# Kernel optimization log

Measured on AMD Instinct MI355X. Metric: run time of the kernel, lower is better.

Reference implementation:

```python
import jax, jax.numpy as jnp
import numpy as np

N, E, G, H, C, DIN, DE = 20000, 320000, 32, 8, 56, 32, 5
HC = H * C  # 448
NEG_SLOPE = 0.2
EPS_BN = 1e-5


def _seg_softmax(scores, seg, num):
    # scores: [E, H], softmax over edges sharing the same target node
    m = jax.ops.segment_max(scores, seg, num_segments=num)
    e = jnp.exp(scores - m[seg])
    s = jax.ops.segment_sum(e, seg, num_segments=num)
    return e / (s[seg] + 1e-16)


def _add_self_loops(src, dst, eattr, n):
    # PyG fill_value='mean': self-loop edge_attr = mean of incoming edge_attr
    deg = jax.ops.segment_sum(jnp.ones((src.shape[0],), eattr.dtype), dst, num_segments=n)
    esum = jax.ops.segment_sum(eattr, dst, num_segments=n)
    loop_attr = esum / jnp.maximum(deg, 1.0)[:, None]
    ar = jnp.arange(n, dtype=src.dtype)
    return (jnp.concatenate([src, ar]), jnp.concatenate([dst, ar]),
            jnp.concatenate([eattr, loop_attr], axis=0))


def _gatv2(x, src, dst, eattr, Wl, Wr, We, att, bias, n):
    xl = (x @ Wl).reshape(n, H, C)  # source transform (messages)
    xr = (x @ Wr).reshape(n, H, C)  # target transform
    ee = (eattr @ We).reshape(-1, H, C)
    s = jax.nn.leaky_relu(xl[src] + xr[dst] + ee, NEG_SLOPE)  # [E, H, C]
    score = jnp.einsum('ehc,hc->eh', s, att)
    alpha = _seg_softmax(score, dst, n)
    out = jax.ops.segment_sum(alpha[..., None] * xl[src], dst, num_segments=n)
    return out.reshape(n, HC) + bias


def _bn(x, gamma, beta):
    m = x.mean(axis=0)
    v = x.var(axis=0)  # biased variance, as torch BatchNorm1d (training)
    return (x - m) * jax.lax.rsqrt(v + EPS_BN) * gamma + beta


def setup_inputs() -> dict:
    key = jax.random.key(0)
    ks = jax.random.split(key, 18)
    sc = lambda k, shape: (jax.random.normal(k, shape, jnp.float32) * 0.05)
    return {
        'x': jax.random.normal(ks[0], (N, DIN), jnp.float32),
        'edge_index': jax.random.randint(ks[1], (2, E), 0, N),
        'edge_attr': jax.random.normal(ks[2], (E, DE), jnp.float32),
        'batch': jnp.sort(jax.random.randint(ks[3], (N,), 0, G)),
        'Wl1': sc(ks[4], (DIN, HC)), 'Wr1': sc(ks[5], (DIN, HC)),
        'We1': sc(ks[6], (DE, HC)), 'att1': sc(ks[7], (H, C)),
        'bias1': jnp.zeros((HC,), jnp.float32),
        'Wl2': sc(ks[8], (HC, HC)), 'Wr2': sc(ks[9], (HC, HC)),
        'We2': sc(ks[10], (DE, HC)), 'att2': sc(ks[11], (H, C)),
        'bias2': jnp.zeros((HC,), jnp.float32),
        'bn_gamma': jnp.ones((HC,), jnp.float32),
        'bn_beta': jnp.zeros((HC,), jnp.float32),
        'Wlin': sc(ks[12], (HC, 18)),
        'blin': jnp.zeros((18,), jnp.float32),
    }


def reference(x, edge_index, edge_attr, batch, Wl1, Wr1, We1, att1, bias1,
              Wl2, Wr2, We2, att2, bias2, bn_gamma, bn_beta, Wlin, blin):
    src, dst = edge_index[0], edge_index[1]
    src2, dst2, ea2 = _add_self_loops(src, dst, edge_attr, N)
    # dropout is identity in eval
    h = _gatv2(x, src2, dst2, ea2, Wl1, Wr1, We1, att1, bias1, N)
    h = jax.nn.elu(h)
    h = _bn(h, bn_gamma, bn_beta)
    h = _gatv2(h, src2, dst2, ea2, Wl2, Wr2, We2, att2, bias2, N)
    # global mean pool per graph
    cnt = jax.ops.segment_sum(jnp.ones((N,), h.dtype), batch, num_segments=G)
    pooled = jax.ops.segment_sum(h, batch, num_segments=G) / jnp.maximum(cnt, 1.0)[:, None]
    pooled = _bn(pooled, bn_gamma, bn_beta)
    logits = pooled @ Wlin + blin
    return jax.nn.log_softmax(logits, axis=1)
```

## Files before the change

kernel.cpp:

```cpp
#include <hip/hip_runtime.h>
#include <hip/hip_bf16.h>

#define NN   20000
#define EE   320000
#define EN   340000
#define HH   8
#define CC   56
#define HC   448
#define DEA  5
#define EAS  8
#define DINN 32
#define GG   32
#define NEG  0.2f

#define SS   896
#define MT   157
#define NT   7

typedef short bf16x8 __attribute__((ext_vector_type(8)));
typedef float f32x4  __attribute__((ext_vector_type(4)));
typedef float f32x8  __attribute__((ext_vector_type(8)));

static __device__ __forceinline__ unsigned short f2bf(float f) {
  unsigned int u = __float_as_uint(f);
  u += 0x7fffu + ((u >> 16) & 1u);
  return (unsigned short)(u >> 16);
}

static __device__ __forceinline__ f32x8 bf8_to_f32x8(uint4 u) {
  f32x8 o;
  o[0] = __uint_as_float(u.x << 16); o[1] = __uint_as_float(u.x & 0xffff0000u);
  o[2] = __uint_as_float(u.y << 16); o[3] = __uint_as_float(u.y & 0xffff0000u);
  o[4] = __uint_as_float(u.z << 16); o[5] = __uint_as_float(u.z & 0xffff0000u);
  o[6] = __uint_as_float(u.w << 16); o[7] = __uint_as_float(u.w & 0xffff0000u);
  return o;
}

static __device__ __forceinline__ float dpp8_sum(float x) {
  int v = __float_as_int(x);
  x += __int_as_float(__builtin_amdgcn_update_dpp(0, v, 0xB1, 0xF, 0xF, true));
  v = __float_as_int(x);
  x += __int_as_float(__builtin_amdgcn_update_dpp(0, v, 0x4E, 0xF, 0xF, true));
  v = __float_as_int(x);
  x += __int_as_float(__builtin_amdgcn_update_dpp(0, v, 0x141, 0xF, 0xF, true));
  return x;
}

__global__ void k_deg(const int* __restrict__ dst, int* deg) {
  int e = blockIdx.x * 256 + threadIdx.x;
  if (e < EE) atomicAdd(&deg[dst[e]], 1);
}

__global__ __launch_bounds__(1024) void k_scan(const int* __restrict__ deg, int* offs,
                                               int* cursor) {
  __shared__ int tot[1024];
  int t = threadIdx.x;
  int base = t * 20;
  int loc[20];
  int s = 0;
  #pragma unroll
  for (int i = 0; i < 20; i++) {
    int idx = base + i;
    int v = (idx < NN) ? deg[idx] + 1 : 0;
    loc[i] = s;
    s += v;
  }
  tot[t] = s;
  __syncthreads();
  for (int o = 1; o < 1024; o <<= 1) {
    int v = (t >= o) ? tot[t - o] : 0;
    __syncthreads();
    tot[t] += v;
    __syncthreads();
  }
  int basesum = (t == 0) ? 0 : tot[t - 1];
  #pragma unroll
  for (int i = 0; i < 20; i++) {
    int idx = base + i;
    if (idx < NN) { offs[idx] = basesum + loc[i]; cursor[idx] = basesum + loc[i]; }
  }
  if (t == 1023) offs[NN] = tot[1023];
}

__global__ void k_scatter(const int* __restrict__ src, const int* __restrict__ dst,
                          const float* __restrict__ ea,
                          int* cursor, int* __restrict__ csr_src, float* __restrict__ csr_ea) {
  int i = blockIdx.x * 256 + threadIdx.x;
  if (i >= EE) return;
  int d = dst[i], s = src[i];
  float a[DEA];
  #pragma unroll
  for (int j = 0; j < DEA; j++) a[j] = ea[(size_t)i * DEA + j];
  int pos = atomicAdd(&cursor[d], 1);
  csr_src[pos] = s;
  float* o = csr_ea + (size_t)pos * EAS;
  *(f32x4*)o       = (f32x4){a[0], a[1], a[2], a[3]};
  *(f32x4*)(o + 4) = (f32x4){a[4], 0.f, 0.f, 0.f};
}

#define XCN (NN * DINN)
#define W1N (SS * DINN)
#define W2N (SS * HC)
__global__ void k_aux(const int* __restrict__ offs,
                      int* __restrict__ csr_src, float* __restrict__ csr_ea,
                      const float* __restrict__ x, unsigned short* __restrict__ xb,
                      const float* __restrict__ Wl1, const float* __restrict__ Wr1,
                      unsigned short* __restrict__ W1t,
                      const float* __restrict__ Wl2, const float* __restrict__ Wr2,
                      unsigned short* __restrict__ W2t) {
  int i = blockIdx.x * 256 + threadIdx.x;
  if (i < NN) {
    int n = i;
    int e0 = offs[n], e1 = offs[n + 1] - 1;
    float a0 = 0.f, a1 = 0.f, a2 = 0.f, a3 = 0.f, a4 = 0.f;
    for (int e = e0; e < e1; e++) {
      const float* p = csr_ea + (size_t)e * EAS;
      a0 += p[0]; a1 += p[1]; a2 += p[2]; a3 += p[3]; a4 += p[4];
    }
    float inv = 1.f / fmaxf((float)(e1 - e0), 1.f);
    csr_src[e1] = n;
    float* o = csr_ea + (size_t)e1 * EAS;
    *(f32x4*)o       = (f32x4){a0 * inv, a1 * inv, a2 * inv, a3 * inv};
    *(f32x4*)(o + 4) = (f32x4){a4 * inv, 0.f, 0.f, 0.f};
    return;
  }
  i -= NN;
  if (i < XCN) { xb[i] = f2bf(x[i]); return; }
  i -= XCN;
  if (i < W1N) {
    int col = i / DINN, k = i - col * DINN;
    int cc = (col < HC) ? col : col - HC;
    const float* W = (col < HC) ? Wl1 : Wr1;
    W1t[i] = f2bf(W[(size_t)k * HC + cc]);
    return;
  }
  i -= W1N;
  if (i < W2N) {
    int col = i / HC, k = i - col * HC;
    int cc = (col < HC) ? col : col - HC;
    const float* W = (col < HC) ? Wl2 : Wr2;
    W2t[i] = f2bf(W[(size_t)k * HC + cc]);
  }
}

__global__ __launch_bounds__(256) void k_gemm1(const unsigned short* __restrict__ xb,
                                               const unsigned short* __restrict__ W1t,
                                               unsigned short* __restrict__ out) {
  int w = threadIdx.x >> 6, lane = threadIdx.x & 63;
  int q = lane >> 4, r = lane & 15;
  int m0 = blockIdx.x * 64;
  int node = blockIdx.y * 64 + w * 16 + r;
  int nc = node < NN ? node : NN - 1;
  bf16x8 b = *(const bf16x8*)(xb + (size_t)nc * DINN + q * 8);
  #pragma unroll
  for (int j = 0; j < 4; j++) {
    bf16x8 a = *(const bf16x8*)(W1t + (size_t)(m0 + j * 16 + r) * DINN + q * 8);
    f32x4 acc = {0.f, 0.f, 0.f, 0.f};
    acc = __builtin_amdgcn_mfma_f32_16x16x32_bf16(a, b, acc, 0, 0, 0);
    uint2 st;
    st.x = ((unsigned int)f2bf(acc[1]) << 16) | f2bf(acc[0]);
    st.y = ((unsigned int)f2bf(acc[3]) << 16) | f2bf(acc[2]);
    if (node < NN)
      *(uint2*)(out + (size_t)node * SS + m0 + j * 16 + q * 4) = st;
  }
}

__global__ __launch_bounds__(256) void k_attn(
    const unsigned short* __restrict__ xlr,
    const int* __restrict__ offs, const int* __restrict__ csr_src,
    const float* __restrict__ csr_ea,
    const float* __restrict__ We, const float* __restrict__ att,
    const float* __restrict__ bias,
    unsigned short* __restrict__ outb, float* __restrict__ outf, int layer1) {
  int n = __builtin_amdgcn_readfirstlane(blockIdx.x * 4 + (threadIdx.x >> 6));
  if (n >= NN) return;
  int lane = threadIdx.x & 63;
  int head = lane >> 3, sub = lane & 7;
  bool v = sub < 7;
  int cb = head * 56 + (v ? sub : 6) * 8;

  f32x8 z = {0.f,0.f,0.f,0.f,0.f,0.f,0.f,0.f};
  f32x8 xr = bf8_to_f32x8(*(const uint4*)(xlr + (size_t)n * SS + HC + cb));
  f32x8 at = *(const f32x8*)(att + cb);
  if (!v) at = z;
  f32x8 w0 = *(const f32x8*)(We + 0 * HC + cb);
  f32x8 w1 = *(const f32x8*)(We + 1 * HC + cb);
  f32x8 w2 = *(const f32x8*)(We + 2 * HC + cb);
  f32x8 w3 = *(const f32x8*)(We + 3 * HC + cb);
  f32x8 w4 = *(const f32x8*)(We + 4 * HC + cb);

  int e0 = offs[n], e1 = offs[n + 1];
  int last = e1 - 1;
  float l = 0.f;
  f32x8 acc = z;

  int s_cur[4];
  #pragma unroll
  for (int k = 0; k < 4; k++) {
    int ek = e0 + k; ek = ek < last ? ek : last;
    s_cur[k] = csr_src[__builtin_amdgcn_readfirstlane(ek)];
  }

  for (int e = e0; e < e1; e += 4) {
    uint4 g[4];
    #pragma unroll
    for (int k = 0; k < 4; k++)
      g[k] = *(const uint4*)(xlr + (size_t)s_cur[k] * SS + cb);

    int en = e + 4;
    if (en < e1) {
      #pragma unroll
      for (int k = 0; k < 4; k++) {
        int ek = en + k; ek = ek < last ? ek : last;
        s_cur[k] = csr_src[__builtin_amdgcn_readfirstlane(ek)];
      }
    }

    f32x8 md[4];
    #pragma unroll
    for (int k = 0; k < 4; k++) {
      int ek = e + k; ek = ek < last ? ek : last;
      md[k] = *(const f32x8*)(csr_ea + (size_t)__builtin_amdgcn_readfirstlane(ek) * EAS);
    }

    #pragma unroll
    for (int k = 0; k < 4; k++) {
      f32x8 tb = xr;
      tb += md[k][0] * w0; tb += md[k][1] * w1; tb += md[k][2] * w2;
      tb += md[k][3] * w3; tb += md[k][4] * w4;
      f32x8 xl = bf8_to_f32x8(g[k]);
      f32x8 t = tb + xl;
      #pragma unroll
      for (int i = 0; i < 8; i++) t[i] = fmaxf(t[i], NEG * t[i]);
      float p = 0.f;
      #pragma unroll
      for (int i = 0; i < 8; i++) p += t[i] * at[i];
      p = dpp8_sum(p);
      float wv = (e + k < e1) ? __expf(fminf(p, 60.f)) : 0.f;
      acc += wv * xl;
      l += wv;
    }
  }

  f32x8 b8 = *(const f32x8*)(bias + cb);
  f32x8 o = acc * (1.f / (l + 1e-16f)) + b8;
  if (layer1) {
    if (v) {
      #pragma unroll
      for (int i = 0; i < 8; i++) o[i] = o[i] > 0.f ? o[i] : (__expf(o[i]) - 1.f);
      uint4 pk;
      pk.x = ((unsigned int)f2bf(o[1]) << 16) | f2bf(o[0]);
      pk.y = ((unsigned int)f2bf(o[3]) << 16) | f2bf(o[2]);
      pk.z = ((unsigned int)f2bf(o[5]) << 16) | f2bf(o[4]);
      pk.w = ((unsigned int)f2bf(o[7]) << 16) | f2bf(o[6]);
      *(uint4*)(outb + (size_t)n * HC + cb) = pk;
    }
  } else if (v) {
    float* dst = outf + (size_t)n * HC + cb;
    *(f32x4*)dst       = (f32x4){o[0], o[1], o[2], o[3]};
    *(f32x4*)(dst + 4) = (f32x4){o[4], o[5], o[6], o[7]};
  }
}

__global__ __launch_bounds__(448) void k_bnstats(const unsigned short* __restrict__ h,
                                                 float* stat) {
  int c = threadIdx.x;
  int rows_per = (NN + gridDim.x - 1) / gridDim.x;
  int r0 = blockIdx.x * rows_per, r1 = min(NN, r0 + rows_per);
  float s = 0.f, sq = 0.f;
  for (int r = r0; r < r1; r++) {
    unsigned int u = h[(size_t)r * HC + c];
    float v = __uint_as_float(u << 16);
    s += v; sq += v * v;
  }
  atomicAdd(&stat[c], s);
  atomicAdd(&stat[HC + c], sq);
}

__global__ __launch_bounds__(64) void k_w2fix(const unsigned short* __restrict__ W2t,
                                              const float* __restrict__ stat,
                                              const float* __restrict__ gam,
                                              const float* __restrict__ bet,
                                              unsigned short* __restrict__ W2s,
                                              float* __restrict__ bias2) {
  int j = blockIdx.x;
  int t = threadIdx.x;
  float bacc = 0.f;
  #pragma unroll
  for (int it = 0; it < 7; it++) {
    int k = t + it * 64;
    float w = __uint_as_float((unsigned int)W2t[(size_t)j * HC + k] << 16);
    float mean = stat[k] * (1.f / NN);
    float var  = stat[HC + k] * (1.f / NN) - mean * mean;
    float sc = rsqrtf(var + 1e-5f) * gam[k];
    float sh = bet[k] - mean * sc;
    bacc += sh * w;
    W2s[(size_t)j * HC + k] = f2bf(sc * w);
  }
  #pragma unroll
  for (int m = 32; m >= 1; m >>= 1) bacc += __shfl_xor(bacc, m, 64);
  if (t == 0) bias2[j] = bacc;
}

__global__ __launch_bounds__(256) void k_gemm2(const unsigned short* __restrict__ A,
                                               const unsigned short* __restrict__ Bt,
                                               const float* __restrict__ bias2,
                                               unsigned short* __restrict__ out) {
  __shared__ unsigned short As[128 * 64];
  __shared__ unsigned short Bs[128 * 64];
  int bid = blockIdx.x;
  int g = bid / 56, rem = bid - g * 56;
  int xs = min(8, MT - g * 8);
  int bx = g * 8 + rem % xs;
  int by = rem / xs;
  int t = threadIdx.x;
  int w = t >> 6, lane = t & 63;
  int wm = w >> 1, wn = w & 1;
  int q = lane >> 4, r = lane & 15;
  int m0 = bx * 128;
  int n0 = by * 128;

  const unsigned short *ag[4], *bg[4];
  unsigned short *la[4], *lb[4];
  #pragma unroll
  for (int j = 0; j < 4; j++) {
    int s = t + j * 256;
    int row = s >> 3;
    int gcol = (s & 7) ^ (row & 7);
    int ar = m0 + row; if (ar >= NN) ar = NN - 1;
    ag[j] = A + (size_t)ar * HC + gcol * 8;
    bg[j] = Bt + (size_t)(n0 + row) * HC + gcol * 8;
    la[j] = As + s * 8;
    lb[j] = Bs + s * 8;
  }

  f32x4 zero = {0.f, 0.f, 0.f, 0.f};
  f32x4 acc[4][4];
  #pragma unroll
  for (int i = 0; i < 4; i++)
    #pragma unroll
    for (int j = 0; j < 4; j++) acc[i][j] = zero;

  for (int k0 = 0; k0 < HC; k0 += 64) {
    #pragma unroll
    for (int j = 0; j < 4; j++) {
      __builtin_amdgcn_global_load_lds(
          (const __attribute__((address_space(1))) unsigned int*)(ag[j] + k0),
          (__attribute__((address_space(3))) unsigned int*)la[j], 16, 0, 0);
      __builtin_amdgcn_global_load_lds(
          (const __attribute__((address_space(1))) unsigned int*)(bg[j] + k0),
          (__attribute__((address_space(3))) unsigned int*)lb[j], 16, 0, 0);
    }
    __syncthreads();
    #pragma unroll
    for (int kk = 0; kk < 64; kk += 32) {
      int p = (kk >> 3) + q;
      bf16x8 af[4], bf[4];
      #pragma unroll
      for (int i = 0; i < 4; i++) {
        int row = wm * 64 + i * 16 + r;
        af[i] = *(const bf16x8*)(As + row * 64 + ((p ^ (r & 7)) * 8));
      }
      #pragma unroll
      for (int j = 0; j < 4; j++) {
        int row = wn * 64 + j * 16 + r;
        bf[j] = *(const bf16x8*)(Bs + row * 64 + ((p ^ (r & 7)) * 8));
      }
      #pragma unroll
      for (int i = 0; i < 4; i++)
        #pragma unroll
        for (int j = 0; j < 4; j++)
          acc[i][j] = __builtin_amdgcn_mfma_f32_16x16x32_bf16(af[i], bf[j], acc[i][j], 0, 0, 0);
    }
    __syncthreads();
  }

  #pragma unroll
  for (int j = 0; j < 4; j++) {
    int col = n0 + wn * 64 + j * 16 + r;
    float bs = bias2[col];
    #pragma unroll
    for (int i = 0; i < 4; i++) {
      int row_base = m0 + wm * 64 + i * 16 + q * 4;
      #pragma unroll
      for (int reg = 0; reg < 4; reg++) {
        int row = row_base + reg;
        if (row < NN) out[(size_t)row * SS + col] = f2bf(acc[i][j][reg] + bs);
      }
    }
  }
}

__global__ __launch_bounds__(448) void k_pool(const float* __restrict__ h2,
                                              const int* __restrict__ batch,
                                              float* pooled, int* cnt) {
  int c = threadIdx.x;
  int rows_per = (NN + gridDim.x - 1) / gridDim.x;
  int r0 = blockIdx.x * rows_per, r1 = min(NN, r0 + rows_per);
  if (r0 >= r1) return;
  float loc = 0.f;
  int rc = 0;
  int gcur = batch[r0];
  for (int r = r0; r < r1; r++) {
    int g = batch[r];
    if (g != gcur) {
      atomicAdd(&pooled[gcur * HC + c], loc);
      if (c == 0) atomicAdd(&cnt[gcur], rc);
      loc = 0.f; rc = 0; gcur = g;
    }
    loc += h2[(size_t)r * HC + c];
    rc++;
  }
  atomicAdd(&pooled[gcur * HC + c], loc);
  if (c == 0) atomicAdd(&cnt[gcur], rc);
}

__global__ __launch_bounds__(448) void k_final(const float* __restrict__ pooled_sum,
                                               const int* __restrict__ cnt,
                                               const float* __restrict__ gam,
                                               const float* __restrict__ bet,
                                               const float* __restrict__ Wlin,
                                               const float* __restrict__ blin,
                                               float* __restrict__ out) {
  __shared__ float P[GG * HC];
  __shared__ float L[GG * 18];
  __shared__ float red[GG];
  int c = threadIdx.x;
  float s = 0.f, sq = 0.f;
  for (int g = 0; g < GG; g++) {
    float v = pooled_sum[g * HC + c] / fmaxf((float)cnt[g], 1.f);
    P[g * HC + c] = v; s += v; sq += v * v;
  }
  float mean = s * (1.f / GG);
  float var  = sq * (1.f / GG) - mean * mean;
  float sc = rsqrtf(var + 1e-5f) * gam[c];
  float sh = bet[c] - mean * sc;
  for (int g = 0; g < GG; g++) P[g * HC + c] = P[g * HC + c] * sc + sh;
  __syncthreads();
  for (int o = c; o < GG * 18; o += HC) {
    int g = o / 18, j = o - g * 18;
    float acc = blin[j];
    for (int k = 0; k < HC; k++) acc += P[g * HC + k] * Wlin[k * 18 + j];
    L[o] = acc;
  }
  __syncthreads();
  if (c < GG) {
    float mx = -3.4e38f;
    for (int j = 0; j < 18; j++) mx = fmaxf(mx, L[c * 18 + j]);
    float se = 0.f;
    for (int j = 0; j < 18; j++) se += __expf(L[c * 18 + j] - mx);
    red[c] = mx + logf(se);
  }
  __syncthreads();
  for (int o = c; o < GG * 18; o += HC) out[o] = L[o] - red[o / 18];
}

extern "C" void kernel_launch(void* const* d_in, const int* in_sizes, int n_in,
                              void* d_out, int out_size, void* d_ws, size_t ws_size,
                              hipStream_t stream) {
  (void)in_sizes; (void)n_in; (void)out_size; (void)ws_size;
  const float* x     = (const float*)d_in[0];
  const int*   ei    = (const int*)d_in[1];
  const float* ea    = (const float*)d_in[2];
  const int*   batch = (const int*)d_in[3];
  const float* Wl1   = (const float*)d_in[4];
  const float* Wr1   = (const float*)d_in[5];
  const float* We1   = (const float*)d_in[6];
  const float* att1  = (const float*)d_in[7];
  const float* bias1 = (const float*)d_in[8];
  const float* Wl2   = (const float*)d_in[9];
  const float* Wr2   = (const float*)d_in[10];
  const float* We2   = (const float*)d_in[11];
  const float* att2  = (const float*)d_in[12];
  const float* bias2in = (const float*)d_in[13];
  const float* gam   = (const float*)d_in[14];
  const float* bet   = (const float*)d_in[15];
  const float* Wlin  = (const float*)d_in[16];
  const float* blin  = (const float*)d_in[17];
  float* out = (float*)d_out;
  const int* srcp = ei;
  const int* dstp = ei + EE;

  char* ws = (char*)d_ws;
  size_t off = 0;
  auto alloc = [&](size_t bytes) -> char* {
    char* p = ws + off;
    off = (off + bytes + 255) & ~(size_t)255;
    return p;
  };
  int*   deg     = (int*)  alloc(NN * 4);
  float* bnstat  = (float*)alloc(HC * 2 * 4);
  float* pooled  = (float*)alloc(GG * HC * 4 + GG * 4);
  int*   cnt     = (int*)(pooled + GG * HC);
  size_t zlen    = (size_t)((char*)(cnt + GG) - (char*)deg);

  int*   offs    = (int*)  alloc((NN + 1) * 4);
  int*   cursor  = (int*)  alloc(NN * 4);
  int*   csr_src = (int*)  alloc((size_t)EN * 4);
  float* csr_ea  = (float*)alloc((size_t)EN * EAS * 4);
  unsigned short* xlr = (unsigned short*)alloc((size_t)NN * SS * 2);
  unsigned short* h1b = (unsigned short*)alloc((size_t)NN * HC * 2);
  float* h1f     = (float*)alloc((size_t)NN * HC * 4);
  unsigned short* xb  = (unsigned short*)alloc((size_t)NN * DINN * 2);
  unsigned short* W1t = (unsigned short*)alloc((size_t)SS * DINN * 2);
  unsigned short* W2t = (unsigned short*)alloc((size_t)SS * HC * 2);
  unsigned short* W2s = (unsigned short*)alloc((size_t)SS * HC * 2);
  float* bias2   = (float*)alloc(SS * 4);

  hipMemsetAsync(deg, 0, zlen, stream);
  k_deg<<<(EE + 255) / 256, 256, 0, stream>>>(dstp, deg);
  k_scan<<<1, 1024, 0, stream>>>(deg, offs, cursor);
  k_scatter<<<(EE + 255) / 256, 256, 0, stream>>>(srcp, dstp, ea, cursor, csr_src, csr_ea);
  k_aux<<<(NN + XCN + W1N + W2N + 255) / 256, 256, 0, stream>>>(
      offs, csr_src, csr_ea, x, xb, Wl1, Wr1, W1t, Wl2, Wr2, W2t);

  dim3 g1(SS / 64, (NN + 63) / 64);
  k_gemm1<<<g1, 256, 0, stream>>>(xb, W1t, xlr);
  k_attn<<<(NN + 3) / 4, 256, 0, stream>>>(xlr, offs, csr_src, csr_ea,
                                           We1, att1, bias1, h1b, h1f, 1);
  k_bnstats<<<512, HC, 0, stream>>>(h1b, bnstat);
  k_w2fix<<<SS, 64, 0, stream>>>(W2t, bnstat, gam, bet, W2s, bias2);

  k_gemm2<<<MT * NT, 256, 0, stream>>>(h1b, W2s, bias2, xlr);
  k_attn<<<(NN + 3) / 4, 256, 0, stream>>>(xlr, offs, csr_src, csr_ea,
                                           We2, att2, bias2in, h1b, h1f, 0);

  k_pool<<<640, HC, 0, stream>>>(h1f, batch, pooled, cnt);
  k_final<<<1, HC, 0, stream>>>(pooled, cnt, gam, bet, Wlin, blin, out);
}
```

Measured before the change: 438.1 us.

## Double-buffer neighbor gathers in GATv2 aggregation loop

Restructures the per-node edge loop into a ping-pong pipeline over two 4-edge batches, so the next batch's source-row gathers and edge-attribute loads are in flight while the current batch computes. Edge attributes are now loaded as a float4 plus one scalar instead of a full 8-float vector. The aim is to hide gather latency. It costs extra registers, and since the average degree is around 17 the prologue may issue wasted clamped loads for low-degree nodes.

```diff
diff --git a/kernel.cpp b/kernel.cpp
--- a/kernel.cpp
+++ b/kernel.cpp
@@ -189,46 +189,59 @@
   f32x8 w3 = *(const f32x8*)(We + 3 * HC + cb);
   f32x8 w4 = *(const f32x8*)(We + 4 * HC + cb);
 
+  const unsigned short* xg = xlr + cb;
+
   int e0 = offs[n], e1 = offs[n + 1];
   int last = e1 - 1;
   float l = 0.f;
   f32x8 acc = z;
 
-  int s_cur[4];
+  int  sA[4], sB[4];
+  uint4 gA[4], gB[4];
+  f32x4 mA[4], mB[4];
+  float m4A[4], m4B[4];
+
   #pragma unroll
   for (int k = 0; k < 4; k++) {
     int ek = e0 + k; ek = ek < last ? ek : last;
-    s_cur[k] = csr_src[__builtin_amdgcn_readfirstlane(ek)];
-  }
-
-  for (int e = e0; e < e1; e += 4) {
-    uint4 g[4];
+    sA[k] = csr_src[__builtin_amdgcn_readfirstlane(ek)];
+  }
+  #pragma unroll
+  for (int k = 0; k < 4; k++)
+    gA[k] = *(const uint4*)(xg + (size_t)sA[k] * SS);
+  #pragma unroll
+  for (int k = 0; k < 4; k++) {
+    int ek = e0 + k; ek = ek < last ? ek : last;
+    const float* p = csr_ea + (size_t)__builtin_amdgcn_readfirstlane(ek) * EAS;
+    mA[k] = *(const f32x4*)p; m4A[k] = p[4];
+  }
+  #pragma unroll
+  for (int k = 0; k < 4; k++) {
+    int ek = e0 + 4 + k; ek = ek < last ? ek : last;
+    sB[k] = csr_src[__builtin_amdgcn_readfirstlane(ek)];
+  }
+
+  for (int e = e0; e < e1; e += 8) {
     #pragma unroll
     for (int k = 0; k < 4; k++)
-      g[k] = *(const uint4*)(xlr + (size_t)s_cur[k] * SS + cb);
-
-    int en = e + 4;
-    if (en < e1) {
-      #pragma unroll
-      for (int k = 0; k < 4; k++) {
-        int ek = en + k; ek = ek < last ? ek : last;
-        s_cur[k] = csr_src[__builtin_amdgcn_readfirstlane(ek)];
-      }
-    }
-
-    f32x8 md[4];
+      gB[k] = *(const uint4*)(xg + (size_t)sB[k] * SS);
     #pragma unroll
     for (int k = 0; k < 4; k++) {
-      int ek = e + k; ek = ek < last ? ek : last;
-      md[k] = *(const f32x8*)(csr_ea + (size_t)__builtin_amdgcn_readfirstlane(ek) * EAS);
-    }
-
+      int ek = e + 4 + k; ek = ek < last ? ek : last;
+      const float* p = csr_ea + (size_t)__builtin_amdgcn_readfirstlane(ek) * EAS;
+      mB[k] = *(const f32x4*)p; m4B[k] = p[4];
+    }
+    #pragma unroll
+    for (int k = 0; k < 4; k++) {
+      int ek = e + 8 + k; ek = ek < last ? ek : last;
+      sA[k] = csr_src[__builtin_amdgcn_readfirstlane(ek)];
+    }
     #pragma unroll
     for (int k = 0; k < 4; k++) {
       f32x8 tb = xr;
-      tb += md[k][0] * w0; tb += md[k][1] * w1; tb += md[k][2] * w2;
-      tb += md[k][3] * w3; tb += md[k][4] * w4;
-      f32x8 xl = bf8_to_f32x8(g[k]);
+      tb += mA[k][0] * w0; tb += mA[k][1] * w1; tb += mA[k][2] * w2;
+      tb += mA[k][3] * w3; tb += m4A[k] * w4;
+      f32x8 xl = bf8_to_f32x8(gA[k]);
       f32x8 t = tb + xl;
       #pragma unroll
       for (int i = 0; i < 8; i++) t[i] = fmaxf(t[i], NEG * t[i]);
@@ -237,6 +250,37 @@
       for (int i = 0; i < 8; i++) p += t[i] * at[i];
       p = dpp8_sum(p);
       float wv = (e + k < e1) ? __expf(fminf(p, 60.f)) : 0.f;
+      acc += wv * xl;
+      l += wv;
+    }
+    #pragma unroll
+    for (int k = 0; k < 4; k++)
+      gA[k] = *(const uint4*)(xg + (size_t)sA[k] * SS);
+    #pragma unroll
+    for (int k = 0; k < 4; k++) {
+      int ek = e + 8 + k; ek = ek < last ? ek : last;
+      const float* p = csr_ea + (size_t)__builtin_amdgcn_readfirstlane(ek) * EAS;
+      mA[k] = *(const f32x4*)p; m4A[k] = p[4];
+    }
+    #pragma unroll
+    for (int k = 0; k < 4; k++) {
+      int ek = e + 12 + k; ek = ek < last ? ek : last;
+      sB[k] = csr_src[__builtin_amdgcn_readfirstlane(ek)];
+    }
+    #pragma unroll
+    for (int k = 0; k < 4; k++) {
+      f32x8 tb = xr;
+      tb += mB[k][0] * w0; tb += mB[k][1] * w1; tb += mB[k][2] * w2;
+      tb += mB[k][3] * w3; tb += m4B[k] * w4;
+      f32x8 xl = bf8_to_f32x8(gB[k]);
+      f32x8 t = tb + xl;
+      #pragma unroll
+      for (int i = 0; i < 8; i++) t[i] = fmaxf(t[i], NEG * t[i]);
+      float p = 0.f;
+      #pragma unroll
+      for (int i = 0; i < 8; i++) p += t[i] * at[i];
+      p = dpp8_sum(p);
+      float wv = (e + 4 + k < e1) ? __expf(fminf(p, 60.f)) : 0.f;
       acc += wv * xl;
       l += wv;
     }
```

After: 440.3 us. No clear change (+0.5%).

## Use packed fp16 math in attention with persistent work-stealing waves

Applied to the files above, without the earlier changes.

Switches the xl/xr projections and edge attributes from bf16/fp32 to fp16, so the attention score can use packed half2 FMAs, with leaky-relu expressed as 0.6t+0.4|t|. It also turns the attention kernel into a persistent grid of 1024 blocks that claim chunks of 4 nodes through an atomic counter, which amortises the per-wave weight setup. The intent is to cut ALU work per edge and launch/setup overhead. The cost is lower precision in the score path and possible fp16 overflow of the projection values.

```diff
diff --git a/kernel.cpp b/kernel.cpp
--- a/kernel.cpp
+++ b/kernel.cpp
@@ -1,5 +1,6 @@
 #include <hip/hip_runtime.h>
 #include <hip/hip_bf16.h>
+#include <hip/hip_fp16.h>
 
 #define NN   20000
 #define EE   320000
@@ -17,6 +18,10 @@
 #define MT   157
 #define NT   7
 
+#define ATT_BLOCKS 1024
+#define ATT_WAVES  (ATT_BLOCKS * 4)
+#define ATT_NB     4
+
 typedef short bf16x8 __attribute__((ext_vector_type(8)));
 typedef float f32x4  __attribute__((ext_vector_type(4)));
 typedef float f32x8  __attribute__((ext_vector_type(8)));
@@ -27,13 +32,19 @@
   return (unsigned short)(u >> 16);
 }
 
-static __device__ __forceinline__ f32x8 bf8_to_f32x8(uint4 u) {
-  f32x8 o;
-  o[0] = __uint_as_float(u.x << 16); o[1] = __uint_as_float(u.x & 0xffff0000u);
-  o[2] = __uint_as_float(u.y << 16); o[3] = __uint_as_float(u.y & 0xffff0000u);
-  o[4] = __uint_as_float(u.z << 16); o[5] = __uint_as_float(u.z & 0xffff0000u);
-  o[6] = __uint_as_float(u.w << 16); o[7] = __uint_as_float(u.w & 0xffff0000u);
-  return o;
+static __device__ __forceinline__ __half2 uash2(unsigned int u) {
+  union { unsigned int u; __half2 h; } c; c.u = u; return c.h;
+}
+static __device__ __forceinline__ unsigned int h2asu(__half2 h) {
+  union { __half2 h; unsigned int u; } c; c.h = h; return c.u;
+}
+static __device__ __forceinline__ __half2 habs2_(__half2 x) {
+  return uash2(h2asu(x) & 0x7fff7fffu);
+}
+static __device__ __forceinline__ unsigned int packh2(float a, float b) {
+  unsigned short l = __half_as_ushort(__float2half_rn(a));
+  unsigned short h = __half_as_ushort(__float2half_rn(b));
+  return ((unsigned int)h << 16) | l;
 }
 
 static __device__ __forceinline__ float dpp8_sum(float x) {
@@ -84,7 +95,8 @@
 
 __global__ void k_scatter(const int* __restrict__ src, const int* __restrict__ dst,
                           const float* __restrict__ ea,
-                          int* cursor, int* __restrict__ csr_src, float* __restrict__ csr_ea) {
+                          int* cursor, int* __restrict__ csr_src,
+                          unsigned int* __restrict__ csr_ea) {
   int i = blockIdx.x * 256 + threadIdx.x;
   if (i >= EE) return;
   int d = dst[i], s = src[i];
@@ -93,16 +105,19 @@
   for (int j = 0; j < DEA; j++) a[j] = ea[(size_t)i * DEA + j];
   int pos = atomicAdd(&cursor[d], 1);
   csr_src[pos] = s;
-  float* o = csr_ea + (size_t)pos * EAS;
-  *(f32x4*)o       = (f32x4){a[0], a[1], a[2], a[3]};
-  *(f32x4*)(o + 4) = (f32x4){a[4], 0.f, 0.f, 0.f};
+  unsigned int pk[DEA];
+  #pragma unroll
+  for (int j = 0; j < DEA; j++) pk[j] = packh2(a[j], a[j]);
+  unsigned int* o = csr_ea + (size_t)pos * EAS;
+  *(uint4*)o       = (uint4){pk[0], pk[1], pk[2], pk[3]};
+  *(uint4*)(o + 4) = (uint4){pk[4], 0u, 0u, 0u};
 }
 
 #define XCN (NN * DINN)
 #define W1N (SS * DINN)
 #define W2N (SS * HC)
 __global__ void k_aux(const int* __restrict__ offs,
-                      int* __restrict__ csr_src, float* __restrict__ csr_ea,
+                      int* __restrict__ csr_src, unsigned int* __restrict__ csr_ea,
                       const float* __restrict__ x, unsigned short* __restrict__ xb,
                       const float* __restrict__ Wl1, const float* __restrict__ Wr1,
                       unsigned short* __restrict__ W1t,
@@ -114,14 +129,19 @@
     int e0 = offs[n], e1 = offs[n + 1] - 1;
     float a0 = 0.f, a1 = 0.f, a2 = 0.f, a3 = 0.f, a4 = 0.f;
     for (int e = e0; e < e1; e++) {
-      const float* p = csr_ea + (size_t)e * EAS;
-      a0 += p[0]; a1 += p[1]; a2 += p[2]; a3 += p[3]; a4 += p[4];
+      const unsigned int* p = csr_ea + (size_t)e * EAS;
+      a0 += __half2float(__ushort_as_half((unsigned short)p[0]));
+      a1 += __half2float(__ushort_as_half((unsigned short)p[1]));
+      a2 += __half2float(__ushort_as_half((unsigned short)p[2]));
+      a3 += __half2float(__ushort_as_half((unsigned short)p[3]));
+      a4 += __half2float(__ushort_as_half((unsigned short)p[4]));
     }
     float inv = 1.f / fmaxf((float)(e1 - e0), 1.f);
     csr_src[e1] = n;
-    float* o = csr_ea + (size_t)e1 * EAS;
-    *(f32x4*)o       = (f32x4){a0 * inv, a1 * inv, a2 * inv, a3 * inv};
-    *(f32x4*)(o + 4) = (f32x4){a4 * inv, 0.f, 0.f, 0.f};
+    unsigned int* o = csr_ea + (size_t)e1 * EAS;
+    *(uint4*)o       = (uint4){packh2(a0 * inv, a0 * inv), packh2(a1 * inv, a1 * inv),
+                               packh2(a2 * inv, a2 * inv), packh2(a3 * inv, a3 * inv)};
+    *(uint4*)(o + 4) = (uint4){packh2(a4 * inv, a4 * inv), 0u, 0u, 0u};
     return;
   }
   i -= NN;
@@ -158,8 +178,8 @@
     f32x4 acc = {0.f, 0.f, 0.f, 0.f};
     acc = __builtin_amdgcn_mfma_f32_16x16x32_bf16(a, b, acc, 0, 0, 0);
     uint2 st;
-    st.x = ((unsigned int)f2bf(acc[1]) << 16) | f2bf(acc[0]);
-    st.y = ((unsigned int)f2bf(acc[3]) << 16) | f2bf(acc[2]);
+    st.x = packh2(acc[0], acc[1]);
+    st.y = packh2(acc[2], acc[3]);
     if (node < NN)
       *(uint2*)(out + (size_t)node * SS + m0 + j * 16 + q * 4) = st;
   }
@@ -168,97 +188,132 @@
 __global__ __launch_bounds__(256) void k_attn(
     const unsigned short* __restrict__ xlr,
     const int* __restrict__ offs, const int* __restrict__ csr_src,
-    const float* __restrict__ csr_ea,
+    const unsigned int* __restrict__ csr_ea,
     const float* __restrict__ We, const float* __restrict__ att,
     const float* __restrict__ bias,
-    unsigned short* __restrict__ outb, float* __restrict__ outf, int layer1) {
-  int n = __builtin_amdgcn_readfirstlane(blockIdx.x * 4 + (threadIdx.x >> 6));
-  if (n >= NN) return;
+    unsigned short* __restrict__ outb, float* __restrict__ outf,
+    int* __restrict__ ctr, int layer1) {
   int lane = threadIdx.x & 63;
   int head = lane >> 3, sub = lane & 7;
   bool v = sub < 7;
   int cb = head * 56 + (v ? sub : 6) * 8;
 
   f32x8 z = {0.f,0.f,0.f,0.f,0.f,0.f,0.f,0.f};
-  f32x8 xr = bf8_to_f32x8(*(const uint4*)(xlr + (size_t)n * SS + HC + cb));
-  f32x8 at = *(const f32x8*)(att + cb);
-  if (!v) at = z;
-  f32x8 w0 = *(const f32x8*)(We + 0 * HC + cb);
-  f32x8 w1 = *(const f32x8*)(We + 1 * HC + cb);
-  f32x8 w2 = *(const f32x8*)(We + 2 * HC + cb);
-  f32x8 w3 = *(const f32x8*)(We + 3 * HC + cb);
-  f32x8 w4 = *(const f32x8*)(We + 4 * HC + cb);
-
-  int e0 = offs[n], e1 = offs[n + 1];
-  int last = e1 - 1;
-  float l = 0.f;
-  f32x8 acc = z;
-
-  int s_cur[4];
-  #pragma unroll
-  for (int k = 0; k < 4; k++) {
-    int ek = e0 + k; ek = ek < last ? ek : last;
-    s_cur[k] = csr_src[__builtin_amdgcn_readfirstlane(ek)];
-  }
-
-  for (int e = e0; e < e1; e += 4) {
-    uint4 g[4];
+  __half2 w0[4], w1[4], w2[4], w3[4], w4[4], at2[4];
+  {
+    f32x8 a = *(const f32x8*)(att + cb);
+    if (!v) a = z;
+    f32x8 W0 = *(const f32x8*)(We + 0 * HC + cb);
+    f32x8 W1 = *(const f32x8*)(We + 1 * HC + cb);
+    f32x8 W2 = *(const f32x8*)(We + 2 * HC + cb);
+    f32x8 W3 = *(const f32x8*)(We + 3 * HC + cb);
+    f32x8 W4 = *(const f32x8*)(We + 4 * HC + cb);
     #pragma unroll
-    for (int k = 0; k < 4; k++)
-      g[k] = *(const uint4*)(xlr + (size_t)s_cur[k] * SS + cb);
-
-    int en = e + 4;
-    if (en < e1) {
+    for (int p = 0; p < 4; p++) {
+      w0[p] = __floats2half2_rn(W0[2*p], W0[2*p+1]);
+      w1[p] = __floats2half2_rn(W1[2*p], W1[2*p+1]);
+      w2[p] = __floats2half2_rn(W2[2*p], W2[2*p+1]);
+      w3[p] = __floats2half2_rn(W3[2*p], W3[2*p+1]);
+      w4[p] = __floats2half2_rn(W4[2*p], W4[2*p+1]);
+      at2[p] = __floats2half2_rn(a[2*p], a[2*p+1]);
+    }
+  }
+  f32x8 b8 = *(const f32x8*)(bias + cb);
+  const __half2 c06 = __float2half2_rn(0.6f);
+  const __half2 c04 = __float2half2_rn(0.4f);
+
+  int wid = __builtin_amdgcn_readfirstlane(blockIdx.x * 4 + (threadIdx.x >> 6));
+  int nbase = wid * ATT_NB;
+
+  while (nbase < NN) {
+    int nend = nbase + ATT_NB; if (nend > NN) nend = NN;
+    for (int n = nbase; n < nend; n++) {
+      uint4 xru = *(const uint4*)(xlr + (size_t)n * SS + HC + cb);
+      __half2 xr2[4] = {uash2(xru.x), uash2(xru.y), uash2(xru.z), uash2(xru.w)};
+
+      int e0 = offs[n], e1 = offs[n + 1], last = e1 - 1;
+      float l = 0.f;
+      f32x8 acc = z;
+
+      int sA[4];
       #pragma unroll
       for (int k = 0; k < 4; k++) {
-        int ek = en + k; ek = ek < last ? ek : last;
-        s_cur[k] = csr_src[__builtin_amdgcn_readfirstlane(ek)];
+        int ek = e0 + k; ek = ek < last ? ek : last;
+        sA[k] = csr_src[ek];
       }
-    }
-
-    f32x8 md[4];
-    #pragma unroll
-    for (int k = 0; k < 4; k++) {
-      int ek = e + k; ek = ek < last ? ek : last;
-      md[k] = *(const f32x8*)(csr_ea + (size_t)__builtin_amdgcn_readfirstlane(ek) * EAS);
-    }
-
-    #pragma unroll
-    for (int k = 0; k < 4; k++) {
-      f32x8 tb = xr;
-      tb += md[k][0] * w0; tb += md[k][1] * w1; tb += md[k][2] * w2;
-      tb += md[k][3] * w3; tb += md[k][4] * w4;
-      f32x8 xl = bf8_to_f32x8(g[k]);
-      f32x8 t = tb + xl;
-      #pragma unroll
-      for (int i = 0; i < 8; i++) t[i] = fmaxf(t[i], NEG * t[i]);
-      float p = 0.f;
-      #pragma unroll
-      for (int i = 0; i < 8; i++) p += t[i] * at[i];
-      p = dpp8_sum(p);
-      float wv = (e + k < e1) ? __expf(fminf(p, 60.f)) : 0.f;
-      acc += wv * xl;
-      l += wv;
-    }
-  }
-
-  f32x8 b8 = *(const f32x8*)(bias + cb);
-  f32x8 o = acc * (1.f / (l + 1e-16f)) + b8;
-  if (layer1) {
-    if (v) {
-      #pragma unroll
-      for (int i = 0; i < 8; i++) o[i] = o[i] > 0.f ? o[i] : (__expf(o[i]) - 1.f);
-      uint4 pk;
-      pk.x = ((unsigned int)f2bf(o[1]) << 16) | f2bf(o[0]);
-      pk.y = ((unsigned int)f2bf(o[3]) << 16) | f2bf(o[2]);
-      pk.z = ((unsigned int)f2bf(o[5]) << 16) | f2bf(o[4]);
-      pk.w = ((unsigned int)f2bf(o[7]) << 16) | f2bf(o[6]);
-      *(uint4*)(outb + (size_t)n * HC + cb) = pk;
-    }
-  } else if (v) {
-    float* dst = outf + (size_t)n * HC + cb;
-    *(f32x4*)dst       = (f32x4){o[0], o[1], o[2], o[3]};
-    *(f32x4*)(dst + 4) = (f32x4){o[4], o[5], o[6], o[7]};
+
+      for (int e = e0; e < e1; e += 4) {
+        uint4 g[4];
+        #pragma unroll
+        for (int k = 0; k < 4; k++)
+          g[k] = *(const uint4*)(xlr + (size_t)sA[k] * SS + cb);
+        int en = e + 4;
+        if (en < e1) {
+          #pragma unroll
+          for (int k = 0; k < 4; k++) {
+            int ek = en + k; ek = ek < last ? ek : last;
+            sA[k] = csr_src[ek];
+          }
+        }
+        uint4 mu[4]; unsigned int m4u[4];
+        #pragma unroll
+        for (int k = 0; k < 4; k++) {
+          int ek = e + k; ek = ek < last ? ek : last;
+          const unsigned int* p = csr_ea + (size_t)ek * EAS;
+          mu[k] = *(const uint4*)p; m4u[k] = p[4];
+        }
+        #pragma unroll
+        for (int k = 0; k < 4; k++) {
+          __half2 a0 = uash2(mu[k].x), a1 = uash2(mu[k].y), a2 = uash2(mu[k].z),
+                  a3 = uash2(mu[k].w), a4 = uash2(m4u[k]);
+          __half2 xl2[4] = {uash2(g[k].x), uash2(g[k].y), uash2(g[k].z), uash2(g[k].w)};
+          __half2 pd = uash2(0u);
+          #pragma unroll
+          for (int p2 = 0; p2 < 4; p2++) {
+            __half2 t = __hfma2(a0, w0[p2], xr2[p2]);
+            t = __hfma2(a1, w1[p2], t);
+            t = __hfma2(a2, w2[p2], t);
+            t = __hfma2(a3, w3[p2], t);
+            t = __hfma2(a4, w4[p2], t);
+            t = __hadd2(t, xl2[p2]);
+            t = __hfma2(c04, habs2_(t), __hmul2(c06, t));
+            pd = __hfma2(t, at2[p2], pd);
+          }
+          float ps = __low2float(pd) + __high2float(pd);
+          ps = dpp8_sum(ps);
+          float wv = (e + k < e1) ? __expf(fminf(ps, 60.f)) : 0.f;
+          #pragma unroll
+          for (int p2 = 0; p2 < 4; p2++) {
+            float2 f = __half22float2(xl2[p2]);
+            acc[2*p2]   += wv * f.x;
+            acc[2*p2+1] += wv * f.y;
+          }
+          l += wv;
+        }
+      }
+
+      f32x8 o = acc * (1.f / (l + 1e-16f)) + b8;
+      if (layer1) {
+        if (v) {
+          #pragma unroll
+          for (int i = 0; i < 8; i++) o[i] = o[i] > 0.f ? o[i] : (__expf(o[i]) - 1.f);
+          uint4 pk;
+          pk.x = ((unsigned int)f2bf(o[1]) << 16) | f2bf(o[0]);
+          pk.y = ((unsigned int)f2bf(o[3]) << 16) | f2bf(o[2]);
+          pk.z = ((unsigned int)f2bf(o[5]) << 16) | f2bf(o[4]);
+          pk.w = ((unsigned int)f2bf(o[7]) << 16) | f2bf(o[6]);
+          *(uint4*)(outb + (size_t)n * HC + cb) = pk;
+        }
+      } else if (v) {
+        float* dst = outf + (size_t)n * HC + cb;
+        *(f32x4*)dst       = (f32x4){o[0], o[1], o[2], o[3]};
+        *(f32x4*)(dst + 4) = (f32x4){o[4], o[5], o[6], o[7]};
+      }
+    }
+    int t;
+    if (lane == 0) t = atomicAdd(ctr, 1);
+    t = __shfl(t, 0, 64);
+    nbase = __builtin_amdgcn_readfirstlane(ATT_WAVES * ATT_NB + t * ATT_NB);
   }
 }
 
@@ -385,7 +440,9 @@
       #pragma unroll
       for (int reg = 0; reg < 4; reg++) {
         int row = row_base + reg;
-        if (row < NN) out[(size_t)row * SS + col] = f2bf(acc[i][j][reg] + bs);
+        if (row < NN)
+          out[(size_t)row * SS + col] =
+              __half_as_ushort(__float2half_rn(acc[i][j][reg] + bs));
       }
     }
   }
@@ -490,14 +547,15 @@
   };
   int*   deg     = (int*)  alloc(NN * 4);
   float* bnstat  = (float*)alloc(HC * 2 * 4);
-  float* pooled  = (float*)alloc(GG * HC * 4 + GG * 4);
+  float* pooled  = (float*)alloc(GG * HC * 4 + GG * 4 + 2 * 4);
   int*   cnt     = (int*)(pooled + GG * HC);
-  size_t zlen    = (size_t)((char*)(cnt + GG) - (char*)deg);
+  int*   attctr  = cnt + GG;
+  size_t zlen    = (size_t)((char*)(attctr + 2) - (char*)deg);
 
   int*   offs    = (int*)  alloc((NN + 1) * 4);
   int*   cursor  = (int*)  alloc(NN * 4);
   int*   csr_src = (int*)  alloc((size_t)EN * 4);
-  float* csr_ea  = (float*)alloc((size_t)EN * EAS * 4);
+  unsigned int* csr_ea = (unsigned int*)alloc((size_t)EN * EAS * 4);
   unsigned short* xlr = (unsigned short*)alloc((size_t)NN * SS * 2);
   unsigned short* h1b = (unsigned short*)alloc((size_t)NN * HC * 2);
   float* h1f     = (float*)alloc((size_t)NN * HC * 4);
@@ -516,14 +574,14 @@
 
   dim3 g1(SS / 64, (NN + 63) / 64);
   k_gemm1<<<g1, 256, 0, stream>>>(xb, W1t, xlr);
-  k_attn<<<(NN + 3) / 4, 256, 0, stream>>>(xlr, offs, csr_src, csr_ea,
-                                           We1, att1, bias1, h1b, h1f, 1);
+  k_attn<<<ATT_BLOCKS, 256, 0, stream>>>(xlr, offs, csr_src, csr_ea,
+                                         We1, att1, bias1, h1b, h1f, attctr, 1);
   k_bnstats<<<512, HC, 0, stream>>>(h1b, bnstat);
   k_w2fix<<<SS, 64, 0, stream>>>(W2t, bnstat, gam, bet, W2s, bias2);
 
   k_gemm2<<<MT * NT, 256, 0, stream>>>(h1b, W2s, bias2, xlr);
-  k_attn<<<(NN + 3) / 4, 256, 0, stream>>>(xlr, offs, csr_src, csr_ea,
-                                           We2, att2, bias2in, h1b, h1f, 0);
+  k_attn<<<ATT_BLOCKS, 256, 0, stream>>>(xlr, offs, csr_src, csr_ea,
+                                         We2, att2, bias2in, h1b, h1f, attctr + 1, 0);
 
   k_pool<<<640, HC, 0, stream>>>(h1f, batch, pooled, cnt);
   k_final<<<1, HC, 0, stream>>>(pooled, cnt, gam, bet, Wlin, blin, out);
```

New measurement: 484.1 us. 10.5% more time.
